# Kernel tuning notes

Hardware: AMD Instinct MI355X
Metric: run time of the kernel (lower is better)

## Reference

```python
import jax, jax.numpy as jnp
import numpy as np

HEADS = 8
K = 3            # kernel_size per axis
RPB = 2 * K - 1  # rel-pos-bias extent per axis
EPS = 1e-5


def _nbr(dim, k):
    # NATTEN-style clamped window: shift window to stay fully inside [0, dim)
    q = jnp.arange(dim)
    start = jnp.clip(q - k // 2, 0, dim - k)
    nbr = start[:, None] + jnp.arange(k)[None, :]       # (dim, k) neighbor coords
    rel = nbr - q[:, None] + (k - 1)                    # (dim, k) in [0, 2k-2]
    return nbr, rel


def _instance_norm(x):
    # InstanceNorm3d, affine=False: normalize over spatial dims per (B, C)
    m = jnp.mean(x, axis=(2, 3, 4), keepdims=True)
    v = jnp.var(x, axis=(2, 3, 4), keepdims=True)
    return (x - m) * jax.lax.rsqrt(v + EPS)


def setup_inputs() -> dict:
    key = jax.random.key(0)
    ks = jax.random.split(key, 10)
    B, C, H, W, Z = 1, 128, 32, 32, 32
    Cf = 4 * C
    s = 0.02
    return {
        "x": jax.random.normal(ks[0], (B, C, H, W, Z), jnp.float32),
        "w_qkv": jax.random.normal(ks[1], (3 * C, C), jnp.float32) * s,
        "b_qkv": jnp.zeros((3 * C,), jnp.float32),
        "rpb": jax.random.normal(ks[2], (HEADS, RPB, RPB, RPB), jnp.float32) * s,
        "w_proj": jax.random.normal(ks[3], (C, C), jnp.float32) * s,
        "b_proj": jnp.zeros((C,), jnp.float32),
        "w_ffn1": jax.random.normal(ks[4], (Cf, C), jnp.float32) * s,
        "b_ffn1": jnp.zeros((Cf,), jnp.float32),
        "w_ffn2": jax.random.normal(ks[5], (C, Cf), jnp.float32) * s,
        "b_ffn2": jnp.zeros((C,), jnp.float32),
    }


def reference(x, w_qkv, b_qkv, rpb, w_proj, b_proj, w_ffn1, b_ffn1, w_ffn2, b_ffn2):
    B, C, H, W, Z = x.shape
    hd = C // HEADS
    N = H * W * Z
    KK = K ** 3

    # ---- SAM: 3D neighborhood self-attention ----
    xt = x.reshape(B, C, N).transpose(0, 2, 1)                 # (B, N, C)
    qkv = xt @ w_qkv.T + b_qkv                                  # (B, N, 3C)
    q, k_, v = jnp.split(qkv, 3, axis=-1)
    split = lambda t: t.reshape(B, N, HEADS, hd).transpose(0, 2, 1, 3)  # (B, h, N, d)
    q, k_, v = split(q), split(k_), split(v)

    nh, rh = _nbr(H, K)
    nw, rw = _nbr(W, K)
    nz, rz = _nbr(Z, K)
    # flat neighbor token index per (h, w, z, kh, kw, kz)
    nbr = ((nh[:, None, None, :, None, None] * W
            + nw[None, :, None, None, :, None]) * Z
           + nz[None, None, :, None, None, :]).reshape(N, KK)   # (N, 27)
    # flat rel-pos-bias index
    bidx = ((rh[:, None, None, :, None, None] * RPB
             + rw[None, :, None, None, :, None]) * RPB
            + rz[None, None, :, None, None, :]).reshape(N, KK)  # (N, 27)

    kg = k_[:, :, nbr]                                          # (B, h, N, 27, d)
    vg = v[:, :, nbr]                                           # (B, h, N, 27, d)
    bias = rpb.reshape(HEADS, RPB ** 3)[:, bidx]                # (h, N, 27)

    scale = jnp.asarray(hd, x.dtype) ** -0.5
    attn = jnp.einsum('bhnd,bhnkd->bhnk', q * scale, kg) + bias
    attn = jax.nn.softmax(attn, axis=-1)
    out = jnp.einsum('bhnk,bhnkd->bhnd', attn, vg)              # (B, h, N, d)
    out = out.transpose(0, 2, 1, 3).reshape(B, N, C) @ w_proj.T + b_proj
    x5 = out.transpose(0, 2, 1).reshape(B, C, H, W, Z)

    # ---- norm_in ----
    x5 = _instance_norm(x5)

    # ---- FFN (mmcv-style, GELU, residual identity) ----
    t = x5.reshape(B, C, N).transpose(0, 2, 1)                  # (B, N, C)
    t = t + (jax.nn.gelu(t @ w_ffn1.T + b_ffn1) @ w_ffn2.T + b_ffn2)
    x5 = t.transpose(0, 2, 1).reshape(B, C, H, W, Z)

    # ---- norm_out ----
    return _instance_norm(x5)
```

## Files before the change

kernel.cpp:

```cpp
#include <hip/hip_runtime.h>
#include <hip/hip_bf16.h>
#include <math.h>

#define NPOS 32768
#define CCH  128
#define C3   384
#define CF   512

typedef __attribute__((ext_vector_type(8))) short short8;
typedef __attribute__((ext_vector_type(4))) float f32x4;

__device__ inline float bf2f(unsigned short u) {
    union { unsigned int i; float f; } x; x.i = ((unsigned int)u) << 16; return x.f;
}
__device__ inline unsigned short f2bf(float f) {
    union { float f; unsigned int i; } x; x.f = f;
    unsigned int r = x.i + 0x7FFFu + ((x.i >> 16) & 1u);
    return (unsigned short)(r >> 16);
}
__device__ inline float lo_bf(unsigned int u) {
    union { unsigned int i; float f; } x; x.i = u << 16; return x.f;
}
__device__ inline float hi_bf(unsigned int u) {
    union { unsigned int i; float f; } x; x.i = u & 0xffff0000u; return x.f;
}

template<bool GELU, bool RES, bool WF32, bool WBF>
__global__ __launch_bounds__(256) void gemm_mfma(
    const unsigned short* __restrict__ A, const unsigned short* __restrict__ B,
    const float* __restrict__ bias, const unsigned short* __restrict__ res,
    float* __restrict__ outf, unsigned short* __restrict__ outb,
    int M, int Nout, int K)
{
    __shared__ alignas(16) unsigned short As[128 * 40];
    __shared__ alignas(16) unsigned short Bs[128 * 40];

    const int tid  = threadIdx.x;
    const int lane = tid & 63;
    const int wave = tid >> 6;
    const int wm = wave & 1, wn = wave >> 1;
    const int row0 = blockIdx.y * 128;
    const int col0 = blockIdx.x * 128;

    const f32x4 fzero = {0.f, 0.f, 0.f, 0.f};
    f32x4 acc[4][4];
    #pragma unroll
    for (int i = 0; i < 4; ++i)
        #pragma unroll
        for (int j = 0; j < 4; ++j) acc[i][j] = fzero;

    const int lr = lane & 15;
    const int lk = (lane >> 4) * 8;

    for (int kt = 0; kt < K; kt += 32) {
        #pragma unroll
        for (int it = 0; it < 2; ++it) {
            const int c = tid + it * 256;
            const int r = c >> 2;
            const int p = (c & 3) * 8;
            *(uint4*)&As[r * 40 + p] = *(const uint4*)&A[(size_t)(row0 + r) * K + kt + p];
            *(uint4*)&Bs[r * 40 + p] = *(const uint4*)&B[(size_t)(col0 + r) * K + kt + p];
        }
        __syncthreads();
        short8 af[4], bfr[4];
        #pragma unroll
        for (int i = 0; i < 4; ++i)
            af[i]  = *(const short8*)&As[(wm * 64 + i * 16 + lr) * 40 + lk];
        #pragma unroll
        for (int j = 0; j < 4; ++j)
            bfr[j] = *(const short8*)&Bs[(wn * 64 + j * 16 + lr) * 40 + lk];
        #pragma unroll
        for (int i = 0; i < 4; ++i)
            #pragma unroll
            for (int j = 0; j < 4; ++j)
                acc[i][j] = __builtin_amdgcn_mfma_f32_16x16x32_bf16(
                                af[i], bfr[j], acc[i][j], 0, 0, 0);
        __syncthreads();
    }

    const int gr0 = row0 + wm * 64 + (lane >> 4) * 4;
    const int gc0 = col0 + wn * 64 + lr;
    #pragma unroll
    for (int j = 0; j < 4; ++j) {
        const int gc = gc0 + j * 16;
        const float bv = bias[gc];
        #pragma unroll
        for (int i = 0; i < 4; ++i) {
            #pragma unroll
            for (int r = 0; r < 4; ++r) {
                const int gr = gr0 + i * 16 + r;
                float v = acc[i][j][r] + bv;
                if (GELU) {
                    const float g = 0.7978845608028654f * (v + 0.044715f * v * v * v);
                    const float e = __expf(2.f * g);
                    v = v * (e / (e + 1.f));
                }
                if (RES)  v += bf2f(res[(size_t)gr * Nout + gc]);
                if (WF32) outf[(size_t)gr * Nout + gc] = v;
                if (WBF)  outb[(size_t)gr * Nout + gc] = f2bf(v);
            }
        }
    }
}

__global__ __launch_bounds__(256) void attn_tiled(
    const unsigned short* __restrict__ qkv, const float* __restrict__ rpb,
    unsigned short* __restrict__ out)
{
    __shared__ unsigned int ksu[288 * 8];
    __shared__ unsigned int vsu[288 * 8];
    __shared__ unsigned int qsu[32 * 8];
    __shared__ float logits[32 * 29];
    __shared__ float rpbs[125];

    const int t  = threadIdx.x;
    const int line = ((blockIdx.x & 7) << 7) + (blockIdx.x >> 3);
    const int h  = blockIdx.y;
    const int w0 = line & 31, h0 = line >> 5;
    const int n0 = (h0 << 10) + (w0 << 5);
    const int sh0 = min(max(h0 - 1, 0), 29);
    const int sw0 = min(max(w0 - 1, 0), 29);
    const int rh_off = sh0 - h0 + 2;
    const int rw_off = sw0 - w0 + 2;

    if (t < 64) {
        const int pos = t >> 1, part = t & 1;
        const uint4 raw = *(const uint4*)&qkv[(size_t)(n0 + pos) * C3 + h * 16 + part * 8];
        *(uint4*)&qsu[pos * 8 + part * 4] = raw;
    } else if (t < 192) {
        const int i = t - 64;
        if (i < 125) rpbs[i] = rpb[h * 125 + i];
    }
    for (int c = t; c < 1152; c += 256) {
        const int p = c >> 2, part = c & 3;
        const int ihw = p >> 5, z = p & 31;
        const int ih = (ihw * 11) >> 5;
        const int iw = ihw - 3 * ih;
        const int n = ((sh0 + ih) << 10) + ((sw0 + iw) << 5) + z;
        const uint4 raw = *(const uint4*)&qkv[(size_t)n * C3 + CCH + (part >> 1) * CCH
                                              + h * 16 + (part & 1) * 8];
        unsigned int* d = ((part < 2) ? ksu : vsu) + p * 8 + (part & 1) * 4;
        *(uint4*)d = raw;
    }
    __syncthreads();

    {
        const int q = t >> 3, j = t & 7;
        const int sz = min(max(q - 1, 0), 29);
        const int rz_off = sz - q + 2;
        float qf[16];
        #pragma unroll
        for (int d2 = 0; d2 < 8; ++d2) {
            const unsigned int u = qsu[q * 8 + d2];
            qf[2 * d2] = lo_bf(u); qf[2 * d2 + 1] = hi_bf(u);
        }
        for (int kk = j; kk < 27; kk += 8) {
            const int ihw = kk / 3, dz = kk - 3 * ihw;
            const int ih = ihw / 3,  iw = ihw - 3 * ih;
            const int p = ihw * 32 + sz + dz;
            float a = 0.f;
            #pragma unroll
            for (int d2 = 0; d2 < 8; ++d2) {
                const unsigned int u = ksu[p * 8 + d2];
                a += qf[2 * d2] * lo_bf(u) + qf[2 * d2 + 1] * hi_bf(u);
            }
            const int bidx = ((ih + rh_off) * 5 + (iw + rw_off)) * 5 + (dz + rz_off);
            logits[q * 29 + kk] = a * 0.25f + rpbs[bidx];
        }
    }
    __syncthreads();

    if (t < 32) {
        float mx = -1e30f;
        #pragma unroll
        for (int kk = 0; kk < 27; ++kk) mx = fmaxf(mx, logits[t * 29 + kk]);
        float s = 0.f;
        #pragma unroll
        for (int kk = 0; kk < 27; ++kk) {
            const float e = __expf(logits[t * 29 + kk] - mx);
            logits[t * 29 + kk] = e; s += e;
        }
        const float inv = 1.f / s;
        #pragma unroll
        for (int kk = 0; kk < 27; ++kk) logits[t * 29 + kk] *= inv;
    }
    __syncthreads();

    {
        const int q = t >> 3, d2 = t & 7;
        const int sz = min(max(q - 1, 0), 29);
        float ax = 0.f, ay = 0.f;
        #pragma unroll
        for (int kk = 0; kk < 27; ++kk) {
            const int p = (kk / 3) * 32 + sz + (kk % 3);
            const float w = logits[q * 29 + kk];
            const unsigned int u = vsu[p * 8 + d2];
            ax += w * lo_bf(u); ay += w * hi_bf(u);
        }
        const unsigned int o = ((unsigned int)f2bf(ay) << 16) | (unsigned int)f2bf(ax);
        *(unsigned int*)&out[(size_t)(n0 + q) * CCH + h * 16 + d2 * 2] = o;
    }
}

__global__ __launch_bounds__(128) void stats_kernel(
    const float* __restrict__ a, float* __restrict__ stats)
{
    const int c = threadIdx.x;
    const int r0 = blockIdx.x * 128;
    float s = 0.f, sq = 0.f;
    for (int r = 0; r < 128; ++r) {
        const float v = a[(size_t)(r0 + r) * CCH + c];
        s += v; sq += v * v;
    }
    atomicAdd(&stats[c], s);
    atomicAdd(&stats[CCH + c], sq);
}

__global__ __launch_bounds__(256) void prep_kernel(
    const float* __restrict__ wq, const float* __restrict__ wp,
    const float* __restrict__ w1, const float* __restrict__ w2,
    unsigned short* __restrict__ wq_b, unsigned short* __restrict__ wp_b,
    unsigned short* __restrict__ w1_b, unsigned short* __restrict__ w2_b,
    float* __restrict__ stats)
{
    const int i = blockIdx.x * 256 + threadIdx.x;
    if (blockIdx.x == 0) {
        stats[threadIdx.x] = 0.f;
        stats[threadIdx.x + 256] = 0.f;
    }
    const float* src; unsigned short* dst; int off;
    if (i < 12288)      { src = wq; dst = wq_b; off = i; }
    else if (i < 16384) { src = wp; dst = wp_b; off = i - 12288; }
    else if (i < 32768) { src = w1; dst = w1_b; off = i - 16384; }
    else                { src = w2; dst = w2_b; off = i - 32768; }
    const float4 v = ((const float4*)src)[off];
    ushort4 o;
    o.x = f2bf(v.x); o.y = f2bf(v.y); o.z = f2bf(v.z); o.w = f2bf(v.w);
    ((ushort4*)dst)[off] = o;
}

__global__ __launch_bounds__(256) void norm_apply_bf(
    const float* __restrict__ a, const float* __restrict__ stats,
    unsigned short* __restrict__ o)
{
    const int i = blockIdx.x * 256 + threadIdx.x;
    const int c0 = (i * 4) & (CCH - 1);
    const float4 v = ((const float4*)a)[i];
    const float invN = 1.f / (float)NPOS;
    ushort4 r;
    #pragma unroll
    for (int j = 0; j < 4; ++j) {
        const int c = c0 + j;
        const float m = stats[c] * invN;
        const float var = stats[CCH + c] * invN - m * m;
        const float rs = rsqrtf(var + 1e-5f);
        (&r.x)[j] = f2bf(((&v.x)[j] - m) * rs);
    }
    *(ushort4*)&o[(size_t)i * 4] = r;
}

__global__ void norm_transpose_kernel(
    const float* __restrict__ t, const float* __restrict__ stats,
    float* __restrict__ out)
{
    __shared__ float tile[32][33];
    const int n0 = blockIdx.x * 32;
    const int c0 = blockIdx.y * 32;
    const int tx = threadIdx.x;
    const int ty = threadIdx.y;
    for (int i = ty; i < 32; i += 8)
        tile[i][tx] = t[(size_t)(n0 + i) * CCH + c0 + tx];
    __syncthreads();
    const float invN = 1.f / (float)NPOS;
    for (int i = ty; i < 32; i += 8) {
        const int c = c0 + i;
        const float m = stats[c] * invN;
        const float var = stats[CCH + c] * invN - m * m;
        const float rs = rsqrtf(var + 1e-5f);
        out[(size_t)c * NPOS + n0 + tx] = (tile[tx][i] - m) * rs;
    }
}

__global__ __launch_bounds__(256) void transpose_x_kernel(
    const float* __restrict__ x, unsigned short* __restrict__ xt)
{
    __shared__ float tile[32][33];
    const int n0 = blockIdx.x * 32;
    const int c0 = blockIdx.y * 32;
    const int tx = threadIdx.x & 31;
    const int ty = threadIdx.x >> 5;
    for (int i = ty; i < 32; i += 8)
        tile[i][tx] = x[(size_t)(c0 + i) * NPOS + n0 + tx];
    __syncthreads();
    for (int i = ty; i < 32; i += 8)
        xt[(size_t)(n0 + i) * CCH + c0 + tx] = f2bf(tile[tx][i]);
}

extern "C" void kernel_launch(void* const* d_in, const int* in_sizes, int n_in,
                              void* d_out, int out_size, void* d_ws, size_t ws_size,
                              hipStream_t stream)
{
    const float* x      = (const float*)d_in[0];
    const float* w_qkv  = (const float*)d_in[1];
    const float* b_qkv  = (const float*)d_in[2];
    const float* rpb    = (const float*)d_in[3];
    const float* w_proj = (const float*)d_in[4];
    const float* b_proj = (const float*)d_in[5];
    const float* w_ffn1 = (const float*)d_in[6];
    const float* b_ffn1 = (const float*)d_in[7];
    const float* w_ffn2 = (const float*)d_in[8];
    const float* b_ffn2 = (const float*)d_in[9];
    float* out = (float*)d_out;

    char* ws = (char*)d_ws;
    unsigned short* xt_bf    = (unsigned short*)(ws + 0);
    unsigned short* qkv_bf   = (unsigned short*)(ws + 8388608);
    unsigned short* ffn1_bf  = (unsigned short*)(ws + 0);
    unsigned short* attnO_bf = (unsigned short*)(ws + 33554432);
    float*          x5       = (float*)(ws + 41943040);
    unsigned short* x5n_bf   = (unsigned short*)(ws + 58720256);
    float*          tbuf     = (float*)(ws + 67108864);
    unsigned short* wqkv_bf  = (unsigned short*)(ws + 83886080);
    unsigned short* wproj_bf = (unsigned short*)(ws + 83984384);
    unsigned short* wffn1_bf = (unsigned short*)(ws + 84017152);
    unsigned short* wffn2_bf = (unsigned short*)(ws + 84148224);
    float*          stats    = (float*)(ws + 84279296);

    prep_kernel<<<192, 256, 0, stream>>>(w_qkv, w_proj, w_ffn1, w_ffn2,
                                         wqkv_bf, wproj_bf, wffn1_bf, wffn2_bf, stats);
    transpose_x_kernel<<<dim3(NPOS / 32, CCH / 32), 256, 0, stream>>>(x, xt_bf);

    gemm_mfma<false, false, false, true><<<dim3(C3 / 128, NPOS / 128), 256, 0, stream>>>(
        xt_bf, wqkv_bf, b_qkv, nullptr, nullptr, qkv_bf, NPOS, C3, CCH);

    attn_tiled<<<dim3(1024, 8), 256, 0, stream>>>(qkv_bf, rpb, attnO_bf);

    gemm_mfma<false, false, true, false><<<dim3(1, NPOS / 128), 256, 0, stream>>>(
        attnO_bf, wproj_bf, b_proj, nullptr, x5, nullptr, NPOS, CCH, CCH);

    stats_kernel<<<256, 128, 0, stream>>>(x5, stats);
    norm_apply_bf<<<(NPOS * CCH / 4) / 256, 256, 0, stream>>>(x5, stats, x5n_bf);

    gemm_mfma<true, false, false, true><<<dim3(CF / 128, NPOS / 128), 256, 0, stream>>>(
        x5n_bf, wffn1_bf, b_ffn1, nullptr, nullptr, ffn1_bf, NPOS, CF, CCH);

    gemm_mfma<false, true, true, false><<<dim3(1, NPOS / 128), 256, 0, stream>>>(
        ffn1_bf, wffn2_bf, b_ffn2, x5n_bf, tbuf, nullptr, NPOS, CCH, CF);

    stats_kernel<<<256, 128, 0, stream>>>(tbuf, stats + 256);
    norm_transpose_kernel<<<dim3(NPOS / 32, CCH / 32), dim3(32, 8), 0, stream>>>(
        tbuf, stats + 256, out);
}
```

Before: 211.7 us.

## Fuse proj+stats, fuse FFN1/GELU/FFN2 with norm and residual, transpose in epilogue

Replaces the proj GEMM, stats, norm-apply, FFN1 GEMM, FFN2 GEMM, stats and norm-transpose chain with three kernels. The proj GEMM now writes bf16 x5 and reduces the per-channel statistics in its epilogue. A fused FFN kernel applies the first instance norm on load, keeps the 512-wide GELU hidden activations in shared memory in 128-column chunks, adds the residual, reduces the second-norm statistics, and writes a channel-major transposed output. This removes the large ffn1 intermediate round-trip through global memory and several launches. In exchange, the FFN kernel uses one block per CU with heavy shared memory, and x5 is now stored in bf16, which reduces precision.

```diff
diff --git a/kernel.cpp b/kernel.cpp
--- a/kernel.cpp
+++ b/kernel.cpp
@@ -202,18 +202,296 @@
     }
 }
 
-__global__ __launch_bounds__(128) void stats_kernel(
-    const float* __restrict__ a, float* __restrict__ stats)
-{
-    const int c = threadIdx.x;
-    const int r0 = blockIdx.x * 128;
-    float s = 0.f, sq = 0.f;
-    for (int r = 0; r < 128; ++r) {
-        const float v = a[(size_t)(r0 + r) * CCH + c];
-        s += v; sq += v * v;
-    }
-    atomicAdd(&stats[c], s);
-    atomicAdd(&stats[CCH + c], sq);
+__global__ __launch_bounds__(256) void proj_stats_kernel(
+    const unsigned short* __restrict__ attnO,
+    const unsigned short* __restrict__ wproj,
+    const float* __restrict__ b_proj,
+    unsigned short* __restrict__ x5b,
+    float* __restrict__ stats)
+{
+    __shared__ alignas(16) unsigned short As[128 * 136];
+    __shared__ alignas(16) unsigned short Bs[128 * 136];
+    __shared__ float red[256];
+
+    const int t    = threadIdx.x;
+    const int lane = t & 63;
+    const int wave = t >> 6;
+    const int wm = wave & 1, wn = wave >> 1;
+    const int lr = lane & 15;
+    const int lg = lane >> 4;
+    const int lk = lg * 8;
+    const int n0 = blockIdx.x * 128;
+
+    red[t] = 0.f;
+    #pragma unroll
+    for (int it = 0; it < 8; ++it) {
+        const int idx = t + it * 256;
+        const int row = idx >> 4, rem = (idx & 15) * 8;
+        *(uint4*)&As[row * 136 + rem] = *(const uint4*)&attnO[(size_t)(n0 + row) * CCH + rem];
+        *(uint4*)&Bs[row * 136 + rem] = *(const uint4*)&wproj[row * CCH + rem];
+    }
+    __syncthreads();
+
+    const f32x4 fzero = {0.f, 0.f, 0.f, 0.f};
+    f32x4 acc[4][4];
+    #pragma unroll
+    for (int i = 0; i < 4; ++i)
+        #pragma unroll
+        for (int j = 0; j < 4; ++j) acc[i][j] = fzero;
+
+    #pragma unroll
+    for (int ks = 0; ks < 4; ++ks) {
+        short8 af[4], bfr[4];
+        #pragma unroll
+        for (int i = 0; i < 4; ++i)
+            af[i]  = *(const short8*)&As[(wm * 64 + i * 16 + lr) * 136 + ks * 32 + lk];
+        #pragma unroll
+        for (int j = 0; j < 4; ++j)
+            bfr[j] = *(const short8*)&Bs[(wn * 64 + j * 16 + lr) * 136 + ks * 32 + lk];
+        #pragma unroll
+        for (int i = 0; i < 4; ++i)
+            #pragma unroll
+            for (int j = 0; j < 4; ++j)
+                acc[i][j] = __builtin_amdgcn_mfma_f32_16x16x32_bf16(
+                                af[i], bfr[j], acc[i][j], 0, 0, 0);
+    }
+
+    #pragma unroll
+    for (int j = 0; j < 4; ++j) {
+        const int gc = wn * 64 + j * 16 + lr;
+        const float bv = b_proj[gc];
+        float s = 0.f, q = 0.f;
+        #pragma unroll
+        for (int i = 0; i < 4; ++i)
+            #pragma unroll
+            for (int r = 0; r < 4; ++r) {
+                const int gr = wm * 64 + i * 16 + lg * 4 + r;
+                const float v = acc[i][j][r] + bv;
+                s += v; q += v * v;
+                x5b[(size_t)(n0 + gr) * CCH + gc] = f2bf(v);
+            }
+        atomicAdd(&red[gc], s);
+        atomicAdd(&red[128 + gc], q);
+    }
+    __syncthreads();
+    if (t < 128) {
+        atomicAdd(&stats[t],       red[t]);
+        atomicAdd(&stats[128 + t], red[128 + t]);
+    }
+}
+
+__global__ __launch_bounds__(256, 1) void ffn_fused_kernel(
+    const unsigned short* __restrict__ x5b,
+    const unsigned short* __restrict__ w1,
+    const float* __restrict__ b1,
+    const unsigned short* __restrict__ w2,
+    const float* __restrict__ b2,
+    float* __restrict__ stats,
+    float* __restrict__ tT)
+{
+    __shared__ alignas(16) unsigned short pool[4 * 17408 + 1024];
+    unsigned short* As  = pool;
+    unsigned short* W1s = pool + 17408;
+    unsigned short* W2s = pool + 2 * 17408;
+    unsigned short* Hs  = pool + 3 * 17408;
+    float* red = (float*)(pool + 4 * 17408);
+    float* ms  = red + 256;
+    float* rss = ms + 128;
+
+    const int t    = threadIdx.x;
+    const int lane = t & 63;
+    const int wave = t >> 6;
+    const int wm = wave & 1, wn = wave >> 1;
+    const int lr = lane & 15;
+    const int lg = lane >> 4;
+    const int lk = lg * 8;
+    const int n0 = blockIdx.x * 128;
+    const float invN = 1.f / (float)NPOS;
+    const f32x4 fzero = {0.f, 0.f, 0.f, 0.f};
+
+    red[t] = 0.f;
+    if (t < 128) {
+        const float m = stats[t] * invN;
+        const float v = stats[128 + t] * invN - m * m;
+        ms[t]  = m;
+        rss[t] = rsqrtf(v + 1e-5f);
+    }
+    uint4 pw1[8], pw2[8];
+    #pragma unroll
+    for (int it = 0; it < 8; ++it) {
+        const int idx = t + it * 256;
+        const int row = idx >> 4, rem = (idx & 15) * 8;
+        pw1[it] = *(const uint4*)&w1[(size_t)row * CCH + rem];
+        pw2[it] = *(const uint4*)&w2[(size_t)row * CF + rem];
+    }
+    __syncthreads();
+
+    #pragma unroll
+    for (int it = 0; it < 8; ++it) {
+        const int idx = t + it * 256;
+        const int row = idx >> 4, c0 = (idx & 15) * 8;
+        uint4 raw = *(const uint4*)&x5b[(size_t)(n0 + row) * CCH + c0];
+        unsigned int u[4] = {raw.x, raw.y, raw.z, raw.w};
+        #pragma unroll
+        for (int p = 0; p < 4; ++p) {
+            const int c = c0 + 2 * p;
+            const float a = (lo_bf(u[p]) - ms[c])     * rss[c];
+            const float b = (hi_bf(u[p]) - ms[c + 1]) * rss[c + 1];
+            u[p] = ((unsigned int)f2bf(b) << 16) | (unsigned int)f2bf(a);
+        }
+        uint4 w; w.x = u[0]; w.y = u[1]; w.z = u[2]; w.w = u[3];
+        *(uint4*)&As[row * 136 + c0] = w;
+    }
+
+    f32x4 acc[4][4];
+    #pragma unroll
+    for (int i = 0; i < 4; ++i)
+        #pragma unroll
+        for (int j = 0; j < 4; ++j) acc[i][j] = fzero;
+
+    #pragma unroll 1
+    for (int cc = 0; cc < 4; ++cc) {
+        #pragma unroll
+        for (int it = 0; it < 8; ++it) {
+            const int idx = t + it * 256;
+            const int row = idx >> 4, rem = (idx & 15) * 8;
+            *(uint4*)&W1s[row * 136 + rem] = pw1[it];
+            *(uint4*)&W2s[row * 136 + rem] = pw2[it];
+        }
+        __syncthreads();
+        if (cc < 3) {
+            #pragma unroll
+            for (int it = 0; it < 8; ++it) {
+                const int idx = t + it * 256;
+                const int row = idx >> 4, rem = (idx & 15) * 8;
+                pw1[it] = *(const uint4*)&w1[(size_t)((cc + 1) * 128 + row) * CCH + rem];
+                pw2[it] = *(const uint4*)&w2[(size_t)row * CF + (cc + 1) * 128 + rem];
+            }
+        }
+        f32x4 hacc[4][4];
+        #pragma unroll
+        for (int i = 0; i < 4; ++i)
+            #pragma unroll
+            for (int j = 0; j < 4; ++j) hacc[i][j] = fzero;
+        #pragma unroll
+        for (int ks = 0; ks < 4; ++ks) {
+            short8 af[4], bfr[4];
+            #pragma unroll
+            for (int i = 0; i < 4; ++i)
+                af[i]  = *(const short8*)&As [(wm * 64 + i * 16 + lr) * 136 + ks * 32 + lk];
+            #pragma unroll
+            for (int j = 0; j < 4; ++j)
+                bfr[j] = *(const short8*)&W1s[(wn * 64 + j * 16 + lr) * 136 + ks * 32 + lk];
+            #pragma unroll
+            for (int i = 0; i < 4; ++i)
+                #pragma unroll
+                for (int j = 0; j < 4; ++j)
+                    hacc[i][j] = __builtin_amdgcn_mfma_f32_16x16x32_bf16(
+                                    af[i], bfr[j], hacc[i][j], 0, 0, 0);
+        }
+        #pragma unroll
+        for (int j = 0; j < 4; ++j) {
+            const int gc = wn * 64 + j * 16 + lr;
+            const float bv = b1[cc * 128 + gc];
+            #pragma unroll
+            for (int i = 0; i < 4; ++i)
+                #pragma unroll
+                for (int r = 0; r < 4; ++r) {
+                    float v = hacc[i][j][r] + bv;
+                    const float g = 0.7978845608028654f * (v + 0.044715f * v * v * v);
+                    const float e = __expf(2.f * g);
+                    v = v * (e / (e + 1.f));
+                    const int gr = wm * 64 + i * 16 + lg * 4 + r;
+                    Hs[gr * 136 + gc] = f2bf(v);
+                }
+        }
+        __syncthreads();
+        #pragma unroll
+        for (int ks = 0; ks < 4; ++ks) {
+            short8 af[4], bfr[4];
+            #pragma unroll
+            for (int i = 0; i < 4; ++i)
+                af[i]  = *(const short8*)&Hs [(wm * 64 + i * 16 + lr) * 136 + ks * 32 + lk];
+            #pragma unroll
+            for (int j = 0; j < 4; ++j)
+                bfr[j] = *(const short8*)&W2s[(wn * 64 + j * 16 + lr) * 136 + ks * 32 + lk];
+            #pragma unroll
+            for (int i = 0; i < 4; ++i)
+                #pragma unroll
+                for (int j = 0; j < 4; ++j)
+                    acc[i][j] = __builtin_amdgcn_mfma_f32_16x16x32_bf16(
+                                    af[i], bfr[j], acc[i][j], 0, 0, 0);
+        }
+        __syncthreads();
+    }
+
+    #pragma unroll
+    for (int j = 0; j < 4; ++j) {
+        const int gc = wn * 64 + j * 16 + lr;
+        const float bv = b2[gc];
+        float s = 0.f, q = 0.f;
+        #pragma unroll
+        for (int i = 0; i < 4; ++i)
+            #pragma unroll
+            for (int r = 0; r < 4; ++r) {
+                const int gr = wm * 64 + i * 16 + lg * 4 + r;
+                const float v = acc[i][j][r] + bv + bf2f(As[gr * 136 + gc]);
+                acc[i][j][r] = v;
+                s += v; q += v * v;
+            }
+        atomicAdd(&red[gc], s);
+        atomicAdd(&red[128 + gc], q);
+    }
+    __syncthreads();
+    if (t < 128) {
+        atomicAdd(&stats[256 + t], red[t]);
+        atomicAdd(&stats[384 + t], red[128 + t]);
+    }
+    __syncthreads();
+
+    float* tr = (float*)(pool + 17408);
+    #pragma unroll
+    for (int j = 0; j < 4; ++j) {
+        const int gc = wn * 64 + j * 16 + lr;
+        #pragma unroll
+        for (int i = 0; i < 4; ++i)
+            #pragma unroll
+            for (int r = 0; r < 4; ++r) {
+                const int gr = wm * 64 + i * 16 + lg * 4 + r;
+                tr[gc * 133 + gr] = acc[i][j][r];
+            }
+    }
+    __syncthreads();
+    #pragma unroll
+    for (int it = 0; it < 16; ++it) {
+        const int idx = t + it * 256;
+        const int c = idx >> 5, ch = (idx & 31) * 4;
+        float4 o4;
+        o4.x = tr[c * 133 + ch + 0];
+        o4.y = tr[c * 133 + ch + 1];
+        o4.z = tr[c * 133 + ch + 2];
+        o4.w = tr[c * 133 + ch + 3];
+        *(float4*)&tT[(size_t)c * NPOS + n0 + ch] = o4;
+    }
+}
+
+__global__ __launch_bounds__(256) void norm2_apply_kernel(
+    const float* __restrict__ tT, const float* __restrict__ stats,
+    float* __restrict__ out)
+{
+    const int i = blockIdx.x * 256 + threadIdx.x;
+    const size_t o = (size_t)i * 4;
+    const int c = (int)(o >> 15);
+    const float invN = 1.f / (float)NPOS;
+    const float m  = stats[256 + c] * invN;
+    const float vr = stats[384 + c] * invN - m * m;
+    const float rs = rsqrtf(vr + 1e-5f);
+    float4 v = ((const float4*)tT)[i];
+    v.x = (v.x - m) * rs;
+    v.y = (v.y - m) * rs;
+    v.z = (v.z - m) * rs;
+    v.w = (v.w - m) * rs;
+    ((float4*)out)[i] = v;
 }
 
 __global__ __launch_bounds__(256) void prep_kernel(
@@ -237,48 +515,6 @@
     ushort4 o;
     o.x = f2bf(v.x); o.y = f2bf(v.y); o.z = f2bf(v.z); o.w = f2bf(v.w);
     ((ushort4*)dst)[off] = o;
-}
-
-__global__ __launch_bounds__(256) void norm_apply_bf(
-    const float* __restrict__ a, const float* __restrict__ stats,
-    unsigned short* __restrict__ o)
-{
-    const int i = blockIdx.x * 256 + threadIdx.x;
-    const int c0 = (i * 4) & (CCH - 1);
-    const float4 v = ((const float4*)a)[i];
-    const float invN = 1.f / (float)NPOS;
-    ushort4 r;
-    #pragma unroll
-    for (int j = 0; j < 4; ++j) {
-        const int c = c0 + j;
-        const float m = stats[c] * invN;
-        const float var = stats[CCH + c] * invN - m * m;
-        const float rs = rsqrtf(var + 1e-5f);
-        (&r.x)[j] = f2bf(((&v.x)[j] - m) * rs);
-    }
-    *(ushort4*)&o[(size_t)i * 4] = r;
-}
-
-__global__ void norm_transpose_kernel(
-    const float* __restrict__ t, const float* __restrict__ stats,
-    float* __restrict__ out)
-{
-    __shared__ float tile[32][33];
-    const int n0 = blockIdx.x * 32;
-    const int c0 = blockIdx.y * 32;
-    const int tx = threadIdx.x;
-    const int ty = threadIdx.y;
-    for (int i = ty; i < 32; i += 8)
-        tile[i][tx] = t[(size_t)(n0 + i) * CCH + c0 + tx];
-    __syncthreads();
-    const float invN = 1.f / (float)NPOS;
-    for (int i = ty; i < 32; i += 8) {
-        const int c = c0 + i;
-        const float m = stats[c] * invN;
-        const float var = stats[CCH + c] * invN - m * m;
-        const float rs = rsqrtf(var + 1e-5f);
-        out[(size_t)c * NPOS + n0 + tx] = (tile[tx][i] - m) * rs;
-    }
 }
 
 __global__ __launch_bounds__(256) void transpose_x_kernel(
@@ -315,11 +551,9 @@
     char* ws = (char*)d_ws;
     unsigned short* xt_bf    = (unsigned short*)(ws + 0);
     unsigned short* qkv_bf   = (unsigned short*)(ws + 8388608);
-    unsigned short* ffn1_bf  = (unsigned short*)(ws + 0);
     unsigned short* attnO_bf = (unsigned short*)(ws + 33554432);
-    float*          x5       = (float*)(ws + 41943040);
-    unsigned short* x5n_bf   = (unsigned short*)(ws + 58720256);
-    float*          tbuf     = (float*)(ws + 67108864);
+    unsigned short* x5_bf    = (unsigned short*)(ws + 41943040);
+    float*          tT       = (float*)(ws + 50331648);
     unsigned short* wqkv_bf  = (unsigned short*)(ws + 83886080);
     unsigned short* wproj_bf = (unsigned short*)(ws + 83984384);
     unsigned short* wffn1_bf = (unsigned short*)(ws + 84017152);
@@ -335,19 +569,11 @@
 
     attn_tiled<<<dim3(1024, 8), 256, 0, stream>>>(qkv_bf, rpb, attnO_bf);
 
-    gemm_mfma<false, false, true, false><<<dim3(1, NPOS / 128), 256, 0, stream>>>(
-        attnO_bf, wproj_bf, b_proj, nullptr, x5, nullptr, NPOS, CCH, CCH);
-
-    stats_kernel<<<256, 128, 0, stream>>>(x5, stats);
-    norm_apply_bf<<<(NPOS * CCH / 4) / 256, 256, 0, stream>>>(x5, stats, x5n_bf);
-
-    gemm_mfma<true, false, false, true><<<dim3(CF / 128, NPOS / 128), 256, 0, stream>>>(
-        x5n_bf, wffn1_bf, b_ffn1, nullptr, nullptr, ffn1_bf, NPOS, CF, CCH);
-
-    gemm_mfma<false, true, true, false><<<dim3(1, NPOS / 128), 256, 0, stream>>>(
-        ffn1_bf, wffn2_bf, b_ffn2, x5n_bf, tbuf, nullptr, NPOS, CCH, CF);
-
-    stats_kernel<<<256, 128, 0, stream>>>(tbuf, stats + 256);
-    norm_transpose_kernel<<<dim3(NPOS / 32, CCH / 32), dim3(32, 8), 0, stream>>>(
-        tbuf, stats + 256, out);
-}
+    proj_stats_kernel<<<NPOS / 128, 256, 0, stream>>>(
+        attnO_bf, wproj_bf, b_proj, x5_bf, stats);
+
+    ffn_fused_kernel<<<NPOS / 128, 256, 0, stream>>>(
+        x5_bf, wffn1_bf, b_ffn1, wffn2_bf, b_ffn2, stats, tT);
+
+    norm2_apply_kernel<<<(NPOS * CCH / 4) / 256, 256, 0, stream>>>(tT, stats, out);
+}
```

Measured after the change: 205.6 us. 2.9% less time.
